# Optimization experiments

Measured on AMD Instinct MI355X. Metric: run time of the kernel, lower is better.

The kernel has to match this reference:

```python
import jax, jax.numpy as jnp
import numpy as np

NQ, NL, QD, LD, H = 100000, 32, 384, 1024, 128
E, E_SEE, E_PRED = 1000000, 750000, 250000
N = NQ + NL
EPS = 1e-5


def _bn(x, g, b):
    # BatchNorm1d in training mode: biased batch statistics over node dim
    mu = x.mean(0)
    var = x.var(0)
    return g * (x - mu) * jax.lax.rsqrt(var + EPS) + b


def _general_conv(x, src, dst, ea, Wm, bm, We, be_):
    # PyG GeneralConv (heads=1, no attention, aggr='add', in==out -> identity skip)
    msg = x[src] @ Wm + bm + ea @ We + be_            # [E_see, H]
    agg = jax.ops.segment_sum(msg, dst, num_segments=N)
    return agg + x


def setup_inputs() -> dict:
    key = jax.random.key(0)
    ks = jax.random.split(key, 20)
    s = lambda fan_in: 1.0 / np.sqrt(fan_in)
    return {
        'query_features': jax.random.normal(ks[0], (NQ, QD), jnp.float32),
        'llm_features': jax.random.normal(ks[1], (NL, LD), jnp.float32),
        'edge_index': jax.random.randint(ks[2], (2, E), 0, N, jnp.int64 if jax.config.jax_enable_x64 else jnp.int32),
        'edge_mask': jax.random.randint(ks[3], (E_PRED,), 0, E),
        'edge_can_see': jax.random.randint(ks[4], (E_SEE,), 0, E),
        'edge_weight': jax.random.uniform(ks[5], (E, 1), jnp.float32),
        'Wq': jax.random.normal(ks[6], (QD, H), jnp.float32) * s(QD),
        'bq': jnp.zeros((H,), jnp.float32),
        'Wl': jax.random.normal(ks[7], (LD, H), jnp.float32) * s(LD),
        'bl': jnp.zeros((H,), jnp.float32),
        'W_em': jax.random.normal(ks[8], (1, 1), jnp.float32),
        'b_em': jnp.zeros((1,), jnp.float32),
        'W1m': jax.random.normal(ks[9], (H, H), jnp.float32) * s(H),
        'b1m': jnp.zeros((H,), jnp.float32),
        'W1e': jax.random.normal(ks[10], (1, H), jnp.float32),
        'b1e': jnp.zeros((H,), jnp.float32),
        'W2m': jax.random.normal(ks[11], (H, H), jnp.float32) * s(H),
        'b2m': jnp.zeros((H,), jnp.float32),
        'W2e': jax.random.normal(ks[12], (1, H), jnp.float32),
        'b2e': jnp.zeros((H,), jnp.float32),
        'g1': jnp.ones((H,), jnp.float32), 'beta1': jnp.zeros((H,), jnp.float32),
        'g2': jnp.ones((H,), jnp.float32), 'beta2': jnp.zeros((H,), jnp.float32),
    }


def reference(query_features, llm_features, edge_index, edge_mask, edge_can_see,
              edge_weight, Wq, bq, Wl, bl, W_em, b_em, W1m, b1m, W1e, b1e,
              W2m, b2m, W2e, b2e, g1, beta1, g2, beta2):
    lrelu = jax.nn.leaky_relu  # slope 0.01 (torch default)
    ei_mask = edge_index[:, edge_can_see]       # [2, E_see]
    ei_pred = edge_index[:, edge_mask]          # [2, E_pred]
    ew = lrelu(edge_weight[edge_can_see] @ W_em + b_em)  # [E_see, 1]
    # feature alignment
    x_ini = jnp.concatenate([query_features @ Wq + bq, llm_features @ Wl + bl], 0)  # [N, H]
    src, dst = ei_mask[0], ei_mask[1]
    x = lrelu(_bn(_general_conv(x_ini, src, dst, ew, W1m, b1m, W1e, b1e), g1, beta1))
    x = _bn(_general_conv(x, src, dst, ew, W2m, b2m, W2e, b2e), g2, beta2)
    edge_predict = jax.nn.sigmoid((x_ini[ei_pred[0]] * x[ei_pred[1]]).mean(-1))  # [E_pred]
    return edge_predict
```

## Files before the change

### kernel.cpp

```cpp
#include <hip/hip_runtime.h>
#include <math.h>

#define NQ 100000
#define NL 32
#define QD 384
#define LD 1024
#define H 128
#define E_TOT 1000000
#define E_SEE 750000
#define E_PRED 250000
#define NN (NQ + NL)
#define EPS 1e-5f

#define NB_SCAN ((NN + 255) / 256)
#define NB_GEMM ((NN + 127) / 128)
#define NB_XINI ((NQ + 127) / 128)


__global__ void k_ew_hist(const int* __restrict__ ecs, const int* __restrict__ EI,
                          const float* __restrict__ ewt, const float* __restrict__ Wem,
                          const float* __restrict__ bem, float* __restrict__ ew,
                          int* __restrict__ cnt) {
  int e = blockIdx.x * 256 + threadIdx.x;
  if (e >= E_SEE) return;
  int idx = ecs[e];
  int d = EI[E_TOT + idx];
  atomicAdd(&cnt[d], 1);
  float w = ewt[idx] * Wem[0] + bem[0];
  ew[e] = w > 0.f ? w : 0.01f * w;
}

__global__ void k_scan_block(const int* __restrict__ cnt, int* __restrict__ bsum) {
  __shared__ int red[256];
  int i = blockIdx.x * 256 + threadIdx.x;
  red[threadIdx.x] = (i < NN) ? cnt[i] : 0;
  __syncthreads();
  for (int s = 128; s > 0; s >>= 1) {
    if (threadIdx.x < s) red[threadIdx.x] += red[threadIdx.x + s];
    __syncthreads();
  }
  if (threadIdx.x == 0) bsum[blockIdx.x] = red[0];
}

__global__ void k_scan_top(const int* __restrict__ bsum, int* __restrict__ boff) {
  __shared__ int buf[2][512];
  int t = threadIdx.x;
  int v = (t < NB_SCAN) ? bsum[t] : 0;
  buf[0][t] = v;
  __syncthreads();
  int src = 0;
  for (int d = 1; d < 512; d <<= 1) {
    int x = buf[src][t];
    if (t >= d) x += buf[src][t - d];
    buf[src ^ 1][t] = x;
    __syncthreads();
    src ^= 1;
  }
  if (t < NB_SCAN) boff[t] = buf[src][t] - v;
}

__global__ void k_scan_write(const int* __restrict__ cnt, const int* __restrict__ boff,
                             int* __restrict__ off) {
  __shared__ int buf[2][256];
  int t = threadIdx.x;
  int i = blockIdx.x * 256 + t;
  int v = (i < NN) ? cnt[i] : 0;
  buf[0][t] = v;
  __syncthreads();
  int src = 0;
  for (int d = 1; d < 256; d <<= 1) {
    int x = buf[src][t];
    if (t >= d) x += buf[src][t - d];
    buf[src ^ 1][t] = x;
    __syncthreads();
    src ^= 1;
  }
  if (i < NN) off[i] = boff[blockIdx.x] + buf[src][t] - v;
  if (i == 0) off[NN] = E_SEE;
}

__global__ void k_fill(const int* __restrict__ ecs, const int* __restrict__ EI,
                       const float* __restrict__ ew, const int* __restrict__ off,
                       int* __restrict__ cur, int* __restrict__ csr_src,
                       float* __restrict__ csr_ew) {
  int e = blockIdx.x * 256 + threadIdx.x;
  if (e >= E_SEE) return;
  int idx = ecs[e];
  int s = EI[idx];
  int d = EI[E_TOT + idx];
  int p = off[d] + atomicAdd(&cur[d], 1);
  csr_src[p] = s;
  csr_ew[p] = ew[e];
}


__global__ __launch_bounds__(256) void k_xini(
    const float* __restrict__ qf, const float* __restrict__ lf,
    const float* __restrict__ Wq, const float* __restrict__ bq,
    const float* __restrict__ Wl, const float* __restrict__ bl,
    float* __restrict__ XINI) {
  if ((int)blockIdx.x < NB_XINI) {
    __shared__ float sA[16][132];
    __shared__ float sB[16][128];
    int tid = threadIdx.x;
    int tx = tid & 15, ty = tid >> 4;
    int rowbase = blockIdx.x * 128;
    float c[8][8];
#pragma unroll
    for (int i = 0; i < 8; i++)
#pragma unroll
      for (int j = 0; j < 8; j++) c[i][j] = 0.f;
    for (int kb = 0; kb < QD; kb += 16) {
#pragma unroll
      for (int p = 0; p < 2; ++p) {
        int f = tid + p * 256;
        int row = f >> 2;
        int kq = (f & 3) << 2;
        int gr = rowbase + row;
        float4 v = make_float4(0.f, 0.f, 0.f, 0.f);
        if (gr < NQ) v = *(const float4*)&qf[(size_t)gr * QD + kb + kq];
        sA[kq + 0][row] = v.x; sA[kq + 1][row] = v.y;
        sA[kq + 2][row] = v.z; sA[kq + 3][row] = v.w;
      }
#pragma unroll
      for (int p = 0; p < 2; ++p) {
        int f = tid + p * 256;
        int k = f >> 5;
        int cq = (f & 31) << 2;
        *(float4*)&sB[k][cq] = *(const float4*)&Wq[(size_t)(kb + k) * H + cq];
      }
      __syncthreads();
#pragma unroll
      for (int k = 0; k < 16; ++k) {
        float4 a0 = *(const float4*)&sA[k][ty * 8];
        float4 a1 = *(const float4*)&sA[k][ty * 8 + 4];
        float4 b0 = *(const float4*)&sB[k][tx * 8];
        float4 b1 = *(const float4*)&sB[k][tx * 8 + 4];
        float av[8] = {a0.x, a0.y, a0.z, a0.w, a1.x, a1.y, a1.z, a1.w};
        float bv[8] = {b0.x, b0.y, b0.z, b0.w, b1.x, b1.y, b1.z, b1.w};
#pragma unroll
        for (int i = 0; i < 8; i++)
#pragma unroll
          for (int j = 0; j < 8; j++) c[i][j] = fmaf(av[i], bv[j], c[i][j]);
      }
      __syncthreads();
    }
    int c0 = tx * 8;
    float4 q0 = *(const float4*)&bq[c0];
    float4 q1 = *(const float4*)&bq[c0 + 4];
    float bb[8] = {q0.x, q0.y, q0.z, q0.w, q1.x, q1.y, q1.z, q1.w};
#pragma unroll
    for (int i = 0; i < 8; i++) {
      int n = rowbase + ty * 8 + i;
      if (n >= NQ) continue;
      float o[8];
#pragma unroll
      for (int j = 0; j < 8; j++) o[j] = c[i][j] + bb[j];
      *(float4*)&XINI[(size_t)n * H + c0] = make_float4(o[0], o[1], o[2], o[3]);
      *(float4*)&XINI[(size_t)n * H + c0 + 4] = make_float4(o[4], o[5], o[6], o[7]);
    }
  } else {
    int r = blockIdx.x - NB_XINI;
    int t = threadIdx.x;
    if (r >= NL || t >= H) return;
    float acc = 0.f;
    for (int k = 0; k < LD; k += 4) {
      float a0 = lf[(size_t)r * LD + k + 0];
      float a1 = lf[(size_t)r * LD + k + 1];
      float a2 = lf[(size_t)r * LD + k + 2];
      float a3 = lf[(size_t)r * LD + k + 3];
      acc = fmaf(a0, Wl[(size_t)(k + 0) * H + t], acc);
      acc = fmaf(a1, Wl[(size_t)(k + 1) * H + t], acc);
      acc = fmaf(a2, Wl[(size_t)(k + 2) * H + t], acc);
      acc = fmaf(a3, Wl[(size_t)(k + 3) * H + t], acc);
    }
    XINI[(size_t)(NQ + r) * H + t] = acc + bl[t];
  }
}


template <bool TRANS>
__global__ __launch_bounds__(256) void k_seg(
    const float* __restrict__ Xin, const int* __restrict__ off,
    const int* __restrict__ csr_src, const float* __restrict__ csr_ew,
    const float* __restrict__ scale, const float* __restrict__ shift,
    float* __restrict__ S, float* __restrict__ swsum, float* __restrict__ degf) {
  int w = blockIdx.x * 4 + (threadIdx.x >> 6);
  if (w >= NN) return;
  int lane = threadIdx.x & 63;
  int o0 = off[w], o1 = off[w + 1];
  float ax = 1.f, ay = 1.f, bx = 0.f, by = 0.f;
  if (TRANS) {
    float2 sc = *(const float2*)&scale[lane * 2];
    float2 sh = *(const float2*)&shift[lane * 2];
    ax = sc.x; ay = sc.y; bx = sh.x; by = sh.y;
  }
  float accx = 0.f, accy = 0.f, ews = 0.f;
  for (int k = o0; k < o1; ++k) {
    int s = csr_src[k];
    float2 v = *(const float2*)&Xin[(size_t)s * H + lane * 2];
    if (TRANS) {
      float t0 = fmaf(ax, v.x, bx); v.x = t0 > 0.f ? t0 : 0.01f * t0;
      float t1 = fmaf(ay, v.y, by); v.y = t1 > 0.f ? t1 : 0.01f * t1;
    }
    accx += v.x; accy += v.y;
    ews += csr_ew[k];
  }
  *(float2*)&S[(size_t)w * H + lane * 2] = make_float2(accx, accy);
  if (lane == 0) { swsum[w] = ews; degf[w] = (float)(o1 - o0); }
}


template <bool TRANS>
__global__ __launch_bounds__(256) void k_gemm(
    const float* __restrict__ S, const float* __restrict__ Xin,
    float* __restrict__ Xout, const float* __restrict__ W,
    const float* __restrict__ bm, const float* __restrict__ be,
    const float* __restrict__ We,
    const float* __restrict__ scale, const float* __restrict__ shift,
    const float* __restrict__ swsum, const float* __restrict__ degf,
    float* __restrict__ partials) {
  __shared__ float sA[16][132];
  __shared__ float sB[16][128];
  __shared__ float st[2][16][128];
  int tid = threadIdx.x;
  int tx = tid & 15, ty = tid >> 4;
  int rowbase = blockIdx.x * 128;
  float c[8][8];
#pragma unroll
  for (int i = 0; i < 8; i++)
#pragma unroll
    for (int j = 0; j < 8; j++) c[i][j] = 0.f;
  for (int kb = 0; kb < H; kb += 16) {
#pragma unroll
    for (int p = 0; p < 2; ++p) {
      int f = tid + p * 256;
      int row = f >> 2;
      int kq = (f & 3) << 2;
      int gr = rowbase + row;
      float4 v = make_float4(0.f, 0.f, 0.f, 0.f);
      if (gr < NN) v = *(const float4*)&S[(size_t)gr * H + kb + kq];
      sA[kq + 0][row] = v.x; sA[kq + 1][row] = v.y;
      sA[kq + 2][row] = v.z; sA[kq + 3][row] = v.w;
    }
#pragma unroll
    for (int p = 0; p < 2; ++p) {
      int f = tid + p * 256;
      int k = f >> 5;
      int cq = (f & 31) << 2;
      *(float4*)&sB[k][cq] = *(const float4*)&W[(size_t)(kb + k) * H + cq];
    }
    __syncthreads();
#pragma unroll
    for (int k = 0; k < 16; ++k) {
      float4 a0 = *(const float4*)&sA[k][ty * 8];
      float4 a1 = *(const float4*)&sA[k][ty * 8 + 4];
      float4 b0 = *(const float4*)&sB[k][tx * 8];
      float4 b1 = *(const float4*)&sB[k][tx * 8 + 4];
      float av[8] = {a0.x, a0.y, a0.z, a0.w, a1.x, a1.y, a1.z, a1.w};
      float bv[8] = {b0.x, b0.y, b0.z, b0.w, b1.x, b1.y, b1.z, b1.w};
#pragma unroll
      for (int i = 0; i < 8; i++)
#pragma unroll
        for (int j = 0; j < 8; j++) c[i][j] = fmaf(av[i], bv[j], c[i][j]);
    }
    __syncthreads();
  }
  int c0 = tx * 8;
  float cb[8], we[8], sc[8], sh[8];
  {
    float4 m0 = *(const float4*)&bm[c0];
    float4 m1 = *(const float4*)&bm[c0 + 4];
    float4 e0 = *(const float4*)&be[c0];
    float4 e1 = *(const float4*)&be[c0 + 4];
    cb[0] = m0.x + e0.x; cb[1] = m0.y + e0.y; cb[2] = m0.z + e0.z; cb[3] = m0.w + e0.w;
    cb[4] = m1.x + e1.x; cb[5] = m1.y + e1.y; cb[6] = m1.z + e1.z; cb[7] = m1.w + e1.w;
    float4 w0 = *(const float4*)&We[c0];
    float4 w1 = *(const float4*)&We[c0 + 4];
    we[0] = w0.x; we[1] = w0.y; we[2] = w0.z; we[3] = w0.w;
    we[4] = w1.x; we[5] = w1.y; we[6] = w1.z; we[7] = w1.w;
    if (TRANS) {
      float4 s0 = *(const float4*)&scale[c0];
      float4 s1 = *(const float4*)&scale[c0 + 4];
      float4 h0 = *(const float4*)&shift[c0];
      float4 h1 = *(const float4*)&shift[c0 + 4];
      sc[0] = s0.x; sc[1] = s0.y; sc[2] = s0.z; sc[3] = s0.w;
      sc[4] = s1.x; sc[5] = s1.y; sc[6] = s1.z; sc[7] = s1.w;
      sh[0] = h0.x; sh[1] = h0.y; sh[2] = h0.z; sh[3] = h0.w;
      sh[4] = h1.x; sh[5] = h1.y; sh[6] = h1.z; sh[7] = h1.w;
    }
  }
  float ps[8], pss[8];
#pragma unroll
  for (int j = 0; j < 8; j++) { ps[j] = 0.f; pss[j] = 0.f; }
#pragma unroll
  for (int i = 0; i < 8; i++) {
    int n = rowbase + ty * 8 + i;
    if (n < NN) {
      float dg = degf[n], sw = swsum[n];
      float4 r0 = *(const float4*)&Xin[(size_t)n * H + c0];
      float4 r1 = *(const float4*)&Xin[(size_t)n * H + c0 + 4];
      float rr[8] = {r0.x, r0.y, r0.z, r0.w, r1.x, r1.y, r1.z, r1.w};
      if (TRANS) {
#pragma unroll
        for (int j = 0; j < 8; j++) {
          float t = fmaf(sc[j], rr[j], sh[j]);
          rr[j] = t > 0.f ? t : 0.01f * t;
        }
      }
      float o[8];
#pragma unroll
      for (int j = 0; j < 8; j++) {
        o[j] = c[i][j] + dg * cb[j] + sw * we[j] + rr[j];
        ps[j] += o[j];
        pss[j] += o[j] * o[j];
      }
      *(float4*)&Xout[(size_t)n * H + c0] = make_float4(o[0], o[1], o[2], o[3]);
      *(float4*)&Xout[(size_t)n * H + c0 + 4] = make_float4(o[4], o[5], o[6], o[7]);
    }
  }
  *(float4*)&st[0][ty][c0] = make_float4(ps[0], ps[1], ps[2], ps[3]);
  *(float4*)&st[0][ty][c0 + 4] = make_float4(ps[4], ps[5], ps[6], ps[7]);
  *(float4*)&st[1][ty][c0] = make_float4(pss[0], pss[1], pss[2], pss[3]);
  *(float4*)&st[1][ty][c0 + 4] = make_float4(pss[4], pss[5], pss[6], pss[7]);
  __syncthreads();
  int stt = tid >> 7, col = tid & 127;
  float s = 0.f;
#pragma unroll
  for (int y = 0; y < 16; y++) s += st[stt][y][col];
  partials[(size_t)blockIdx.x * 256 + tid] = s;
}


__global__ void k_bnstats(const float* __restrict__ partials,
                          const float* __restrict__ g, const float* __restrict__ beta,
                          float* __restrict__ scale, float* __restrict__ shift) {
  __shared__ float s[256];
  int t = threadIdx.x;
  float acc = 0.f;
  for (int b = 0; b < NB_GEMM; ++b) acc += partials[(size_t)b * 256 + t];
  s[t] = acc;
  __syncthreads();
  if (t < H) {
    float mean = s[t] / (float)NN;
    float var = s[128 + t] / (float)NN - mean * mean;
    float a = g[t] * rsqrtf(var + EPS);
    scale[t] = a;
    shift[t] = beta[t] - mean * a;
  }
}


__global__ __launch_bounds__(256) void k_pred(
    const int* __restrict__ emask, const int* __restrict__ EI,
    const float* __restrict__ XINI, const float* __restrict__ X,
    const float* __restrict__ scale, const float* __restrict__ shift,
    float* __restrict__ out) {
  int i = blockIdx.x * 4 + (threadIdx.x >> 6);
  if (i >= E_PRED) return;
  int lane = threadIdx.x & 63;
  int m = emask[i];
  int p0 = EI[m];
  int p1 = EI[E_TOT + m];
  float2 a = *(const float2*)&XINI[(size_t)p0 * H + lane * 2];
  float2 b = *(const float2*)&X[(size_t)p1 * H + lane * 2];
  float2 sc = *(const float2*)&scale[lane * 2];
  float2 sh = *(const float2*)&shift[lane * 2];
  float v = a.x * fmaf(sc.x, b.x, sh.x) + a.y * fmaf(sc.y, b.y, sh.y);
#pragma unroll
  for (int mm = 32; mm > 0; mm >>= 1) v += __shfl_xor(v, mm, 64);
  if (lane == 0) out[i] = 1.f / (1.f + expf(-v * (1.f / 128.f)));
}


extern "C" void kernel_launch(void* const* d_in, const int* in_sizes, int n_in,
                              void* d_out, int out_size, void* d_ws, size_t ws_size,
                              hipStream_t stream) {
  const float* qf    = (const float*)d_in[0];
  const float* lf    = (const float*)d_in[1];
  const int*   EI    = (const int*)d_in[2];
  const int*   emask = (const int*)d_in[3];
  const int*   ecs   = (const int*)d_in[4];
  const float* ewt   = (const float*)d_in[5];
  const float* Wq    = (const float*)d_in[6];
  const float* bq    = (const float*)d_in[7];
  const float* Wl    = (const float*)d_in[8];
  const float* bl    = (const float*)d_in[9];
  const float* Wem   = (const float*)d_in[10];
  const float* bem   = (const float*)d_in[11];
  const float* W1m   = (const float*)d_in[12];
  const float* b1m   = (const float*)d_in[13];
  const float* W1e   = (const float*)d_in[14];
  const float* b1e   = (const float*)d_in[15];
  const float* W2m   = (const float*)d_in[16];
  const float* b2m   = (const float*)d_in[17];
  const float* W2e   = (const float*)d_in[18];
  const float* b2e   = (const float*)d_in[19];
  const float* g1    = (const float*)d_in[20];
  const float* beta1 = (const float*)d_in[21];
  const float* g2    = (const float*)d_in[22];
  const float* beta2 = (const float*)d_in[23];
  float* out = (float*)d_out;

  char* p = (char*)d_ws;
  auto alloc = [&](size_t bytes) -> void* {
    void* r = (void*)p;
    p += (bytes + 255) & ~(size_t)255;
    return r;
  };
  float* XINI    = (float*)alloc((size_t)NN * H * 4);
  float* X       = (float*)alloc((size_t)NN * H * 4);
  float* S       = (float*)alloc((size_t)NN * H * 4);
  float* ew      = (float*)alloc((size_t)E_SEE * 4);
  float* csr_ew  = (float*)alloc((size_t)E_SEE * 4);
  int*   csr_src = (int*)alloc((size_t)E_SEE * 4);
  int*   cnt     = (int*)alloc((size_t)NN * 4);
  int*   off     = (int*)alloc((size_t)(NN + 1) * 4);
  int*   cur     = (int*)alloc((size_t)NN * 4);
  int*   bsum    = (int*)alloc((size_t)NB_SCAN * 4);
  int*   boff    = (int*)alloc((size_t)NB_SCAN * 4);
  float* swsum   = (float*)alloc((size_t)NN * 4);
  float* degf    = (float*)alloc((size_t)NN * 4);
  float* partials= (float*)alloc((size_t)NB_GEMM * 256 * 4);
  float* scale1  = (float*)alloc(128 * 4);
  float* shift1  = (float*)alloc(128 * 4);
  float* scale2  = (float*)alloc(128 * 4);
  float* shift2  = (float*)alloc(128 * 4);

  hipMemsetAsync(cnt, 0, (size_t)NN * 4, stream);
  hipMemsetAsync(cur, 0, (size_t)NN * 4, stream);

  int ebl = (E_SEE + 255) / 256;
  k_ew_hist<<<ebl, 256, 0, stream>>>(ecs, EI, ewt, Wem, bem, ew, cnt);
  k_scan_block<<<NB_SCAN, 256, 0, stream>>>(cnt, bsum);
  k_scan_top<<<1, 512, 0, stream>>>(bsum, boff);
  k_scan_write<<<NB_SCAN, 256, 0, stream>>>(cnt, boff, off);
  k_fill<<<ebl, 256, 0, stream>>>(ecs, EI, ew, off, cur, csr_src, csr_ew);

  k_xini<<<NB_XINI + NL, 256, 0, stream>>>(qf, lf, Wq, bq, Wl, bl, XINI);

  int segbl = (NN + 3) / 4;
  k_seg<false><<<segbl, 256, 0, stream>>>(XINI, off, csr_src, csr_ew,
                                          nullptr, nullptr, S, swsum, degf);
  k_gemm<false><<<NB_GEMM, 256, 0, stream>>>(S, XINI, X, W1m, b1m, b1e, W1e,
                                             nullptr, nullptr, swsum, degf, partials);
  k_bnstats<<<1, 256, 0, stream>>>(partials, g1, beta1, scale1, shift1);
  k_seg<true><<<segbl, 256, 0, stream>>>(X, off, csr_src, csr_ew,
                                         scale1, shift1, S, swsum, degf);
  k_gemm<true><<<NB_GEMM, 256, 0, stream>>>(S, X, X, W2m, b2m, b2e, W2e,
                                            scale1, shift1, swsum, degf, partials);
  k_bnstats<<<1, 256, 0, stream>>>(partials, g2, beta2, scale2, shift2);
  int pbl = (E_PRED + 3) / 4;
  k_pred<<<pbl, 256, 0, stream>>>(emask, EI, XINI, X, scale2, shift2, out);
}
```

Before: 849.9 us.

## Compute query feature projection with bf16 MFMA instead of fp32 FMA tiles

Replaces the fp32 register-tiled FMA GEMM for query_features @ Wq with a bf16 MFMA (16x16x32) kernel. Activations are rounded to bf16 on the fly into shared memory, and Wq is pre-transposed and converted to bf16 by a new prep kernel. The aim is to use the matrix cores for this 100k x 384 x 128 GEMM. The cost is lower precision in x_ini, which feeds both the message passing and the final prediction, and the output stores are now scalar rather than float4.

```diff
diff --git a/kernel.cpp b/kernel.cpp
--- a/kernel.cpp
+++ b/kernel.cpp
@@ -15,6 +15,16 @@
 #define NB_SCAN ((NN + 255) / 256)
 #define NB_GEMM ((NN + 127) / 128)
 #define NB_XINI ((NQ + 127) / 128)
+
+typedef __attribute__((ext_vector_type(8))) short short8;
+typedef __attribute__((ext_vector_type(4))) short short4v;
+typedef __attribute__((ext_vector_type(4))) float f32x4;
+
+__device__ __forceinline__ unsigned short f2bf(float f) {
+  unsigned int u = __builtin_bit_cast(unsigned int, f);
+  u = (u + 0x7FFFu + ((u >> 16) & 1u)) >> 16;
+  return (unsigned short)u;
+}
 
 
 __global__ void k_ew_hist(const int* __restrict__ ecs, const int* __restrict__ EI,
@@ -94,70 +104,80 @@
 }
 
 
+__global__ void k_prep_wqt(const float* __restrict__ Wq, unsigned short* __restrict__ Wqt) {
+  for (int i = blockIdx.x * 256 + threadIdx.x; i < QD * H; i += gridDim.x * 256) {
+    int n = i / QD, k = i - n * QD;
+    Wqt[i] = f2bf(Wq[(size_t)k * H + n]);
+  }
+}
+
+
 __global__ __launch_bounds__(256) void k_xini(
     const float* __restrict__ qf, const float* __restrict__ lf,
-    const float* __restrict__ Wq, const float* __restrict__ bq,
+    const unsigned short* __restrict__ Wqt, const float* __restrict__ bq,
     const float* __restrict__ Wl, const float* __restrict__ bl,
     float* __restrict__ XINI) {
   if ((int)blockIdx.x < NB_XINI) {
-    __shared__ float sA[16][132];
-    __shared__ float sB[16][128];
+    __shared__ unsigned short sA[128][40];
+    __shared__ unsigned short sB[128][40];
     int tid = threadIdx.x;
-    int tx = tid & 15, ty = tid >> 4;
+    int w = tid >> 6, lane = tid & 63;
+    int l15 = lane & 15, quad = lane >> 4;
+    int wr = (w >> 1) * 64, wc = (w & 1) * 64;
     int rowbase = blockIdx.x * 128;
-    float c[8][8];
-#pragma unroll
-    for (int i = 0; i < 8; i++)
-#pragma unroll
-      for (int j = 0; j < 8; j++) c[i][j] = 0.f;
-    for (int kb = 0; kb < QD; kb += 16) {
-#pragma unroll
-      for (int p = 0; p < 2; ++p) {
-        int f = tid + p * 256;
-        int row = f >> 2;
-        int kq = (f & 3) << 2;
+    f32x4 acc[4][4];
+#pragma unroll
+    for (int i = 0; i < 4; i++)
+#pragma unroll
+      for (int j = 0; j < 4; j++) acc[i][j] = (f32x4){0.f, 0.f, 0.f, 0.f};
+
+    for (int kb = 0; kb < QD; kb += 32) {
+#pragma unroll
+      for (int pass = 0; pass < 4; ++pass) {
+        int row = pass * 32 + (tid >> 3);
+        int kc = (tid & 7) * 4;
         int gr = rowbase + row;
         float4 v = make_float4(0.f, 0.f, 0.f, 0.f);
-        if (gr < NQ) v = *(const float4*)&qf[(size_t)gr * QD + kb + kq];
-        sA[kq + 0][row] = v.x; sA[kq + 1][row] = v.y;
-        sA[kq + 2][row] = v.z; sA[kq + 3][row] = v.w;
+        if (gr < NQ) v = *(const float4*)&qf[(size_t)gr * QD + kb + kc];
+        short4v b;
+        b.x = (short)f2bf(v.x); b.y = (short)f2bf(v.y);
+        b.z = (short)f2bf(v.z); b.w = (short)f2bf(v.w);
+        *(short4v*)&sA[row][kc] = b;
       }
 #pragma unroll
-      for (int p = 0; p < 2; ++p) {
-        int f = tid + p * 256;
-        int k = f >> 5;
-        int cq = (f & 31) << 2;
-        *(float4*)&sB[k][cq] = *(const float4*)&Wq[(size_t)(kb + k) * H + cq];
+      for (int pass = 0; pass < 2; ++pass) {
+        int n = pass * 64 + (tid >> 2);
+        int k8 = (tid & 3) * 8;
+        *(int4*)&sB[n][k8] = *(const int4*)&Wqt[(size_t)n * QD + kb + k8];
       }
       __syncthreads();
-#pragma unroll
-      for (int k = 0; k < 16; ++k) {
-        float4 a0 = *(const float4*)&sA[k][ty * 8];
-        float4 a1 = *(const float4*)&sA[k][ty * 8 + 4];
-        float4 b0 = *(const float4*)&sB[k][tx * 8];
-        float4 b1 = *(const float4*)&sB[k][tx * 8 + 4];
-        float av[8] = {a0.x, a0.y, a0.z, a0.w, a1.x, a1.y, a1.z, a1.w};
-        float bv[8] = {b0.x, b0.y, b0.z, b0.w, b1.x, b1.y, b1.z, b1.w};
-#pragma unroll
-        for (int i = 0; i < 8; i++)
-#pragma unroll
-          for (int j = 0; j < 8; j++) c[i][j] = fmaf(av[i], bv[j], c[i][j]);
+      short8 af[4], bfr[4];
+#pragma unroll
+      for (int mt = 0; mt < 4; ++mt)
+        af[mt] = *(const short8*)&sA[wr + mt * 16 + l15][quad * 8];
+#pragma unroll
+      for (int nt = 0; nt < 4; ++nt)
+        bfr[nt] = *(const short8*)&sB[wc + nt * 16 + l15][quad * 8];
+#pragma unroll
+      for (int mt = 0; mt < 4; ++mt)
+#pragma unroll
+        for (int nt = 0; nt < 4; ++nt)
+          acc[mt][nt] = __builtin_amdgcn_mfma_f32_16x16x32_bf16(
+              af[mt], bfr[nt], acc[mt][nt], 0, 0, 0);
+      __syncthreads();
+    }
+#pragma unroll
+    for (int nt = 0; nt < 4; ++nt) {
+      int col = wc + nt * 16 + l15;
+      float bias = bq[col];
+#pragma unroll
+      for (int mt = 0; mt < 4; ++mt) {
+#pragma unroll
+        for (int r = 0; r < 4; ++r) {
+          int n = rowbase + wr + mt * 16 + quad * 4 + r;
+          if (n < NQ) XINI[(size_t)n * H + col] = acc[mt][nt][r] + bias;
+        }
       }
-      __syncthreads();
-    }
-    int c0 = tx * 8;
-    float4 q0 = *(const float4*)&bq[c0];
-    float4 q1 = *(const float4*)&bq[c0 + 4];
-    float bb[8] = {q0.x, q0.y, q0.z, q0.w, q1.x, q1.y, q1.z, q1.w};
-#pragma unroll
-    for (int i = 0; i < 8; i++) {
-      int n = rowbase + ty * 8 + i;
-      if (n >= NQ) continue;
-      float o[8];
-#pragma unroll
-      for (int j = 0; j < 8; j++) o[j] = c[i][j] + bb[j];
-      *(float4*)&XINI[(size_t)n * H + c0] = make_float4(o[0], o[1], o[2], o[3]);
-      *(float4*)&XINI[(size_t)n * H + c0 + 4] = make_float4(o[4], o[5], o[6], o[7]);
     }
   } else {
     int r = blockIdx.x - NB_XINI;
@@ -426,18 +446,20 @@
   float* shift1  = (float*)alloc(128 * 4);
   float* scale2  = (float*)alloc(128 * 4);
   float* shift2  = (float*)alloc(128 * 4);
+  unsigned short* Wqt = (unsigned short*)alloc((size_t)QD * H * 2);
 
   hipMemsetAsync(cnt, 0, (size_t)NN * 4, stream);
   hipMemsetAsync(cur, 0, (size_t)NN * 4, stream);
 
   int ebl = (E_SEE + 255) / 256;
+  k_prep_wqt<<<48, 256, 0, stream>>>(Wq, Wqt);
   k_ew_hist<<<ebl, 256, 0, stream>>>(ecs, EI, ewt, Wem, bem, ew, cnt);
   k_scan_block<<<NB_SCAN, 256, 0, stream>>>(cnt, bsum);
   k_scan_top<<<1, 512, 0, stream>>>(bsum, boff);
   k_scan_write<<<NB_SCAN, 256, 0, stream>>>(cnt, boff, off);
   k_fill<<<ebl, 256, 0, stream>>>(ecs, EI, ew, off, cur, csr_src, csr_ew);
 
-  k_xini<<<NB_XINI + NL, 256, 0, stream>>>(qf, lf, Wq, bq, Wl, bl, XINI);
+  k_xini<<<NB_XINI + NL, 256, 0, stream>>>(qf, lf, Wqt, bq, Wl, bl, XINI);
 
   int segbl = (NN + 3) / 4;
   k_seg<false><<<segbl, 256, 0, stream>>>(XINI, off, csr_src, csr_ew,
```

Result: faster. 825.1 us (-2.9%).
